# Kernel tuning notes

Measured on AMD Instinct MI355X. Metric: run time of the kernel, lower is better.

The kernel has to match this reference:

```python
import jax, jax.numpy as jnp
import numpy as np

# tree structure: B trees, layer sizes per tree 2048 -> 256 -> 32 -> 1 (arities 8, 8, 32)
B = 256
N0, N1, N2, N3 = B * 2048, B * 256, B * 32, B * 1
D_IN, HID, OUT = 128, 256, 10
EPS = 1e-5


def _bn(x, g, b):
    # BatchNorm1d, training-mode batch stats (biased variance), as in torch
    mu = jnp.mean(x, axis=0)
    var = jnp.var(x, axis=0)
    return (x - mu) * jax.lax.rsqrt(var + EPS) * g + b


def _tree_layer(pooled, w1, b1, bn1g, bn1b, w2, b2, bng, bnb):
    # MLP(2 layers): Linear -> BN -> ReLU -> Linear, then outer BN -> ReLU (next_layer)
    z = jax.nn.relu(_bn(pooled @ w1 + b1, bn1g, bn1b))
    z = z @ w2 + b2
    return jax.nn.relu(_bn(z, bng, bnb))


def setup_inputs() -> dict:
    key = jax.random.key(0)
    ks = jax.random.split(key, 12)
    s = 0.05
    ar = lambda n: jnp.arange(n, dtype=jnp.int32)
    inp = {
        'x': jax.random.normal(ks[0], (N0, D_IN), jnp.float32),
        # child -> parent index (global, trees are contiguous blocks)
        'parent1': ar(N0) // 8,
        'parent2': ar(N1) // 8,
        'parent3': ar(N2) // 32,
        # node -> tree id per layer (for sum tree-pooling readout)
        'tree0': ar(N0) // 2048,
        'tree1': ar(N1) // 256,
        'tree2': ar(N2) // 32,
        # layer 1 MLP (input_dim -> hidden)
        'l1_w1': jax.random.normal(ks[1], (D_IN, HID), jnp.float32) * s,
        'l1_b1': jnp.zeros((HID,), jnp.float32),
        'l1_bn1g': jnp.ones((HID,), jnp.float32),
        'l1_bn1b': jnp.zeros((HID,), jnp.float32),
        'l1_w2': jax.random.normal(ks[2], (HID, HID), jnp.float32) * s,
        'l1_b2': jnp.zeros((HID,), jnp.float32),
        'l1_bng': jnp.ones((HID,), jnp.float32),
        'l1_bnb': jnp.zeros((HID,), jnp.float32),
        # layers 2 and 3 MLPs (hidden -> hidden), stacked on axis 0
        'lw1': jax.random.normal(ks[3], (2, HID, HID), jnp.float32) * s,
        'lb1': jnp.zeros((2, HID), jnp.float32),
        'lbn1g': jnp.ones((2, HID), jnp.float32),
        'lbn1b': jnp.zeros((2, HID), jnp.float32),
        'lw2': jax.random.normal(ks[4], (2, HID, HID), jnp.float32) * s,
        'lb2': jnp.zeros((2, HID), jnp.float32),
        'lbng': jnp.ones((2, HID), jnp.float32),
        'lbnb': jnp.zeros((2, HID), jnp.float32),
        # prediction heads
        'pred0_w': jax.random.normal(ks[5], (D_IN, OUT), jnp.float32) * s,
        'pred0_b': jnp.zeros((OUT,), jnp.float32),
        'predh_w': jax.random.normal(ks[6], (3, HID, OUT), jnp.float32) * s,
        'predh_b': jnp.zeros((3, OUT), jnp.float32),
    }
    return inp


def reference(x, parent1, parent2, parent3, tree0, tree1, tree2,
              l1_w1, l1_b1, l1_bn1g, l1_bn1b, l1_w2, l1_b2, l1_bng, l1_bnb,
              lw1, lb1, lbn1g, lbn1b, lw2, lb2, lbng, lbnb,
              pred0_w, pred0_b, predh_w, predh_b):
    seg = jax.ops.segment_sum
    h0 = x
    # layer 1: sparse child pooling (spmm == segment_sum) + MLP + BN + ReLU
    h1 = _tree_layer(seg(h0, parent1, num_segments=N1),
                     l1_w1, l1_b1, l1_bn1g, l1_bn1b, l1_w2, l1_b2, l1_bng, l1_bnb)
    h2 = _tree_layer(seg(h1, parent2, num_segments=N2),
                     lw1[0], lb1[0], lbn1g[0], lbn1b[0], lw2[0], lb2[0], lbng[0], lbnb[0])
    h3 = _tree_layer(seg(h2, parent3, num_segments=N3),
                     lw1[1], lb1[1], lbn1g[1], lbn1b[1], lw2[1], lb2[1], lbng[1], lbnb[1])
    # sum tree-pooling readout over layers 0..depth-1, plus root-layer linear
    score = seg(h0, tree0, num_segments=B) @ pred0_w + pred0_b
    score = score + seg(h1, tree1, num_segments=B) @ predh_w[0] + predh_b[0]
    score = score + seg(h2, tree2, num_segments=B) @ predh_w[1] + predh_b[1]
    score = score + h3 @ predh_w[2] + predh_b[2]  # h3 has 1 root per tree -> [B, OUT]
    return score
```

## Files before the change

kernel.cpp:

```cpp
#include <hip/hip_runtime.h>
#include <hip/hip_bf16.h>


#define N0 (256*2048)
#define N1 (256*256)
#define N2 (256*32)
#define NB 256
#define BN_EPS 1e-5f

typedef __attribute__((ext_vector_type(8))) __bf16 bf16x8;
typedef __attribute__((ext_vector_type(8))) unsigned short u16x8;
typedef __attribute__((ext_vector_type(4))) unsigned short u16x4;
typedef __attribute__((ext_vector_type(4))) float f32x4;

__device__ inline float bf2f(unsigned short b) {
    unsigned u = ((unsigned)b) << 16;
    float f; __builtin_memcpy(&f, &u, 4); return f;
}
__device__ inline unsigned short f2bf(float f) {
    unsigned u; __builtin_memcpy(&u, &f, 4);
    u += 0x7fff + ((u >> 16) & 1);
    return (unsigned short)(u >> 16);
}

__global__ __launch_bounds__(256) void prep_weights(const float* __restrict__ l1_w1,
                                                    const float* __restrict__ l1_w2,
                                                    const float* __restrict__ lw1,
                                                    const float* __restrict__ lw2,
                                                    unsigned short* __restrict__ Wt) {
    int idx = blockIdx.x * 256 + threadIdx.x;
    if (idx >= 360448) return;
    float v;
    if (idx < 32768) {
        int n = idx >> 7, k = idx & 127;
        v = l1_w1[k * 256 + n];
    } else if (idx < 98304) {
        int j = idx - 32768, n = j >> 8, k = j & 255;
        v = l1_w2[k * 256 + n];
    } else if (idx < 163840) {
        int j = idx - 98304, n = j >> 8, k = j & 255;
        v = lw1[k * 256 + n];
    } else if (idx < 229376) {
        int j = idx - 163840, n = j >> 8, k = j & 255;
        v = lw2[k * 256 + n];
    } else if (idx < 294912) {
        int j = idx - 229376, n = j >> 8, k = j & 255;
        v = lw1[65536 + k * 256 + n];
    } else {
        int j = idx - 294912, n = j >> 8, k = j & 255;
        v = lw2[65536 + k * 256 + n];
    }
    Wt[idx] = f2bf(v);
}

__global__ __launch_bounds__(256) void pool8_128(const float* __restrict__ x,
                                                 unsigned short* __restrict__ out) {
    int v = blockIdx.x * 256 + threadIdx.x;
    int c4 = v & 31, p = v >> 5;
    const f32x4* xp = reinterpret_cast<const f32x4*>(x + (size_t)p * 8 * 128 + c4 * 4);
    f32x4 s = {0.f, 0.f, 0.f, 0.f};
#pragma unroll
    for (int c = 0; c < 8; ++c) s += xp[c * 32];
    u16x4 o;
#pragma unroll
    for (int e = 0; e < 4; ++e) o[e] = f2bf(s[e]);
    *reinterpret_cast<u16x4*>(out + (size_t)p * 128 + c4 * 4) = o;
}

template <int ROWS, int D>
__global__ void treesum_bf(const unsigned short* __restrict__ in, float* __restrict__ out) {
    int t = blockIdx.x, d = threadIdx.x;
    const unsigned short* p = in + (size_t)t * ROWS * D + d;
    float s = 0.f;
    for (int r = 0; r < ROWS; ++r) s += bf2f(p[(size_t)r * D]);
    out[t * D + d] = s;
}

template <int GROUP>
__global__ __launch_bounds__(256) void pool_bn_relu(const unsigned short* __restrict__ Z,
                                                    const float* __restrict__ scale,
                                                    const float* __restrict__ shift,
                                                    unsigned short* __restrict__ out) {
    int v = blockIdx.x * 256 + threadIdx.x;
    int c8 = v & 31, p = v >> 5;
    int d0 = c8 * 8;
    float sc[8], sh[8], s[8];
#pragma unroll
    for (int e = 0; e < 8; ++e) { sc[e] = scale[d0 + e]; sh[e] = shift[d0 + e]; s[e] = 0.f; }
#pragma unroll
    for (int g = 0; g < GROUP; ++g) {
        u16x8 z = *reinterpret_cast<const u16x8*>(Z + ((size_t)p * GROUP + g) * 256 + d0);
#pragma unroll
        for (int e = 0; e < 8; ++e) {
            float f = sc[e] * bf2f(z[e]) + sh[e];
            s[e] += f > 0.f ? f : 0.f;
        }
    }
    u16x8 o;
#pragma unroll
    for (int e = 0; e < 8; ++e) o[e] = f2bf(s[e]);
    *reinterpret_cast<u16x8*>(out + (size_t)p * 256 + d0) = o;
}

__global__ void bn_finalize(const float* __restrict__ partials,
                            const float* __restrict__ g, const float* __restrict__ b,
                            float invM, float* __restrict__ ss ) {
    int d = threadIdx.x;
    float s = 0.f, s2 = 0.f;
    for (int slot = 0; slot < 32; ++slot) {
        s  += partials[slot * 512 + d];
        s2 += partials[slot * 512 + 256 + d];
    }
    float mean = s * invM;
    float var = s2 * invM - mean * mean;
    float sc = g[d] * rsqrtf(var + BN_EPS);
    ss[d] = sc;
    ss[256 + d] = b[d] - mean * sc;
}

template <int KD, bool BN_A>
__global__ __launch_bounds__(256) void mfma_gemm(const unsigned short* __restrict__ A,
                                                 const float* __restrict__ scale,
                                                 const float* __restrict__ shift,
                                                 const unsigned short* __restrict__ Wt,
                                                 const float* __restrict__ bias,
                                                 unsigned short* __restrict__ C,
                                                 float* __restrict__ stat_partials) {
    constexpr int LDA = 72;
    __shared__ unsigned short Asb[64 * LDA];
    __shared__ unsigned short Bsb[256 * LDA];
    const int m0 = blockIdx.x * 64;
    const int tid = threadIdx.x;
    const int wave = tid >> 6, lane = tid & 63;
    const int q = lane >> 4, r = lane & 15;

    f32x4 acc[4][4];
#pragma unroll
    for (int i = 0; i < 4; ++i)
#pragma unroll
        for (int j = 0; j < 4; ++j) acc[i][j] = (f32x4){0.f, 0.f, 0.f, 0.f};

    for (int k0 = 0; k0 < KD; k0 += 64) {
#pragma unroll
        for (int i = 0; i < 2; ++i) {
            int v = tid + i * 256;
            int row = v >> 3, kc = v & 7;
            u16x8 d = *reinterpret_cast<const u16x8*>(A + (size_t)(m0 + row) * KD + k0 + kc * 8);
            if (BN_A) {
                u16x8 o;
#pragma unroll
                for (int e = 0; e < 8; ++e) {
                    int k = k0 + kc * 8 + e;
                    float f = scale[k] * bf2f(d[e]) + shift[k];
                    o[e] = f2bf(f > 0.f ? f : 0.f);
                }
                d = o;
            }
            *reinterpret_cast<u16x8*>(&Asb[row * LDA + kc * 8]) = d;
        }
#pragma unroll
        for (int i = 0; i < 8; ++i) {
            int v = tid + i * 256;
            int n = v >> 3, kc = v & 7;
            u16x8 d = *reinterpret_cast<const u16x8*>(Wt + (size_t)n * KD + k0 + kc * 8);
            *reinterpret_cast<u16x8*>(&Bsb[n * LDA + kc * 8]) = d;
        }
        __syncthreads();
#pragma unroll
        for (int s = 0; s < 2; ++s) {
            bf16x8 a[4], b[4];
#pragma unroll
            for (int i = 0; i < 4; ++i)
                a[i] = *reinterpret_cast<const bf16x8*>(&Asb[(i * 16 + r) * LDA + s * 32 + q * 8]);
#pragma unroll
            for (int j = 0; j < 4; ++j)
                b[j] = *reinterpret_cast<const bf16x8*>(&Bsb[(wave * 64 + j * 16 + r) * LDA + s * 32 + q * 8]);
#pragma unroll
            for (int i = 0; i < 4; ++i)
#pragma unroll
                for (int j = 0; j < 4; ++j)
                    acc[i][j] = __builtin_amdgcn_mfma_f32_16x16x32_bf16(a[i], b[j], acc[i][j], 0, 0, 0);
        }
        __syncthreads();
    }

    const int col_base = wave * 64;
    float sj[4], s2j[4];
#pragma unroll
    for (int j = 0; j < 4; ++j) {
        float bj = bias[col_base + j * 16 + r];
        float s = 0.f, s2 = 0.f;
#pragma unroll
        for (int i = 0; i < 4; ++i)
#pragma unroll
            for (int e = 0; e < 4; ++e) {
                acc[i][j][e] += bj;
                float v = acc[i][j][e];
                s += v; s2 += v * v;
            }
        s  += __shfl_xor(s, 16);  s  += __shfl_xor(s, 32);
        s2 += __shfl_xor(s2, 16); s2 += __shfl_xor(s2, 32);
        sj[j] = s; s2j[j] = s2;
    }
#pragma unroll
    for (int i = 0; i < 4; ++i)
#pragma unroll
        for (int e = 0; e < 4; ++e) {
            size_t row = m0 + i * 16 + q * 4 + e;
#pragma unroll
            for (int j = 0; j < 4; ++j)
                C[row * 256 + col_base + j * 16 + r] = f2bf(acc[i][j][e]);
        }
    if (q == 0) {
        int slot = blockIdx.x & 31;
#pragma unroll
        for (int j = 0; j < 4; ++j) {
            int col = col_base + j * 16 + r;
            atomicAdd(&stat_partials[slot * 512 + col], sj[j]);
            atomicAdd(&stat_partials[slot * 512 + 256 + col], s2j[j]);
        }
    }
}

__global__ __launch_bounds__(256) void head_kernel(const float* __restrict__ ts0,
                                                   const float* __restrict__ ts1,
                                                   const unsigned short* __restrict__ p3,
                                                   const unsigned short* __restrict__ Z3b,
                                                   const float* __restrict__ ss5,
                                                   const float* __restrict__ p0w,
                                                   const float* __restrict__ p0b,
                                                   const float* __restrict__ phw,
                                                   const float* __restrict__ phb,
                                                   float* __restrict__ out) {
    int t = blockIdx.x, d = threadIdx.x;
    float acc[10];
#pragma unroll
    for (int o = 0; o < 10; ++o) acc[o] = 0.f;
    if (d < 128) {
        float v = ts0[t * 128 + d];
#pragma unroll
        for (int o = 0; o < 10; ++o) acc[o] += v * p0w[d * 10 + o];
    }
    {
        float v = ts1[t * 256 + d];
#pragma unroll
        for (int o = 0; o < 10; ++o) acc[o] += v * phw[d * 10 + o];
    }
    {
        float v = bf2f(p3[t * 256 + d]);
#pragma unroll
        for (int o = 0; o < 10; ++o) acc[o] += v * phw[2560 + d * 10 + o];
    }
    {
        float v = ss5[d] * bf2f(Z3b[t * 256 + d]) + ss5[256 + d];
        v = v > 0.f ? v : 0.f;
#pragma unroll
        for (int o = 0; o < 10; ++o) acc[o] += v * phw[5120 + d * 10 + o];
    }
    __shared__ float red[256];
    for (int o = 0; o < 10; ++o) {
        red[d] = acc[o];
        __syncthreads();
        for (int s = 128; s > 0; s >>= 1) {
            if (d < s) red[d] += red[d + s];
            __syncthreads();
        }
        if (d == 0) out[t * 10 + o] = red[0] + p0b[o] + phb[o] + phb[10 + o] + phb[20 + o];
        __syncthreads();
    }
}

extern "C" void kernel_launch(void* const* d_in, const int* in_sizes, int n_in,
                              void* d_out, int out_size, void* d_ws, size_t ws_size,
                              hipStream_t stream) {
    const float* x       = (const float*)d_in[0];
    const float* l1_w1   = (const float*)d_in[7];
    const float* l1_b1   = (const float*)d_in[8];
    const float* l1_bn1g = (const float*)d_in[9];
    const float* l1_bn1b = (const float*)d_in[10];
    const float* l1_w2   = (const float*)d_in[11];
    const float* l1_b2   = (const float*)d_in[12];
    const float* l1_bng  = (const float*)d_in[13];
    const float* l1_bnb  = (const float*)d_in[14];
    const float* lw1     = (const float*)d_in[15];
    const float* lb1     = (const float*)d_in[16];
    const float* lbn1g   = (const float*)d_in[17];
    const float* lbn1b   = (const float*)d_in[18];
    const float* lw2     = (const float*)d_in[19];
    const float* lb2     = (const float*)d_in[20];
    const float* lbng    = (const float*)d_in[21];
    const float* lbnb    = (const float*)d_in[22];
    const float* pred0_w = (const float*)d_in[23];
    const float* pred0_b = (const float*)d_in[24];
    const float* predh_w = (const float*)d_in[25];
    const float* predh_b = (const float*)d_in[26];
    float* out = (float*)d_out;

    uint8_t* wsb = (uint8_t*)d_ws;
    unsigned short* pooled1 = (unsigned short*)(wsb);
    unsigned short* Z1      = (unsigned short*)(wsb + (16ull << 20));
    unsigned short* Z2      = (unsigned short*)(wsb + (48ull << 20));
    unsigned short* pooled2 = (unsigned short*)(wsb + (80ull << 20));
    unsigned short* Z2a     = (unsigned short*)(wsb + (84ull << 20));
    unsigned short* Z2b     = (unsigned short*)(wsb + (88ull << 20));
    unsigned short* pooled3 = (unsigned short*)(wsb + (92ull << 20));
    unsigned short* Z3a     = (unsigned short*)(wsb + (92ull << 20) + 131072);
    unsigned short* Z3b     = (unsigned short*)(wsb + (92ull << 20) + 262144);
    unsigned short* Wt      = (unsigned short*)(wsb + (93ull << 20));
    float* ts0   = (float*)(wsb + (94ull << 20));
    float* ts1   = (float*)(wsb + (94ull << 20) + 131072);
    float* stats = (float*)(wsb + (95ull << 20));

    auto SP = [&](int i) { return stats + i * 16384; };
    float* ssbase = stats + 6 * 16384;
    auto SS = [&](int i) { return ssbase + i * 512; };

    hipMemsetAsync(stats, 0, 6 * 16384 * sizeof(float), stream);
    prep_weights<<<1408, 256, 0, stream>>>(l1_w1, l1_w2, lw1, lw2, Wt);

    pool8_128<<<N1 * 32 / 256, 256, 0, stream>>>(x, pooled1);
    treesum_bf<256, 128><<<NB, 128, 0, stream>>>(pooled1, ts0);
    mfma_gemm<128, false><<<N1 / 64, 256, 0, stream>>>(pooled1, nullptr, nullptr,
                                                       Wt, l1_b1, Z1, SP(0));
    bn_finalize<<<1, 256, 0, stream>>>(SP(0), l1_bn1g, l1_bn1b, 1.f / N1, SS(0));
    mfma_gemm<256, true><<<N1 / 64, 256, 0, stream>>>(Z1, SS(0), SS(0) + 256,
                                                      Wt + 32768, l1_b2, Z2, SP(1));
    bn_finalize<<<1, 256, 0, stream>>>(SP(1), l1_bng, l1_bnb, 1.f / N1, SS(1));
    pool_bn_relu<8><<<N2 * 32 / 256, 256, 0, stream>>>(Z2, SS(1), SS(1) + 256, pooled2);
    treesum_bf<32, 256><<<NB, 256, 0, stream>>>(pooled2, ts1);

    mfma_gemm<256, false><<<N2 / 64, 256, 0, stream>>>(pooled2, nullptr, nullptr,
                                                       Wt + 98304, lb1, Z2a, SP(2));
    bn_finalize<<<1, 256, 0, stream>>>(SP(2), lbn1g, lbn1b, 1.f / N2, SS(2));
    mfma_gemm<256, true><<<N2 / 64, 256, 0, stream>>>(Z2a, SS(2), SS(2) + 256,
                                                      Wt + 163840, lb2, Z2b, SP(3));
    bn_finalize<<<1, 256, 0, stream>>>(SP(3), lbng, lbnb, 1.f / N2, SS(3));
    pool_bn_relu<32><<<NB * 32 / 256, 256, 0, stream>>>(Z2b, SS(3), SS(3) + 256, pooled3);

    mfma_gemm<256, false><<<NB / 64, 256, 0, stream>>>(pooled3, nullptr, nullptr,
                                                       Wt + 229376, lb1 + 256, Z3a, SP(4));
    bn_finalize<<<1, 256, 0, stream>>>(SP(4), lbn1g + 256, lbn1b + 256, 1.f / NB, SS(4));
    mfma_gemm<256, true><<<NB / 64, 256, 0, stream>>>(Z3a, SS(4), SS(4) + 256,
                                                      Wt + 294912, lb2 + 256, Z3b, SP(5));
    bn_finalize<<<1, 256, 0, stream>>>(SP(5), lbng + 256, lbnb + 256, 1.f / NB, SS(5));

    head_kernel<<<NB, 256, 0, stream>>>(ts0, ts1, pooled3, Z3b, SS(5),
                                        pred0_w, pred0_b, predh_w, predh_b, out);
}
```

Baseline: 190.3 us.

## Fuse BN finalize and tree-sum readouts into neighbouring kernels, retile big GEMMs

Removes the separate bn_finalize launches by recomputing scale/shift from partial stats in each consumer kernel's prologue, and folds the per-tree sum readouts into the pooling kernels using block reductions plus atomics. The stat partial slots are reduced from 32 to 8 so the prologue reads less. The layer-1 GEMMs use 128-row tiles with 512 threads to reuse the weight tile across more rows. This trades fewer launches and passes for redundant per-block BN finalize work and more atomic contention.

```diff
diff --git a/kernel.cpp b/kernel.cpp
--- a/kernel.cpp
+++ b/kernel.cpp
@@ -7,6 +7,7 @@
 #define N2 (256*32)
 #define NB 256
 #define BN_EPS 1e-5f
+#define NSLOT 8
 
 typedef __attribute__((ext_vector_type(8))) __bf16 bf16x8;
 typedef __attribute__((ext_vector_type(8))) unsigned short u16x8;
@@ -53,10 +54,31 @@
     Wt[idx] = f2bf(v);
 }
 
+__device__ inline void bn_prologue(int tid, const float* __restrict__ partials,
+                                   const float* __restrict__ g, const float* __restrict__ b,
+                                   float invM, float* sc_lds, float* sh_lds) {
+    if (tid < 256) {
+        float s = 0.f, s2 = 0.f;
+#pragma unroll
+        for (int k = 0; k < NSLOT; ++k) {
+            s  += partials[k * 512 + tid];
+            s2 += partials[k * 512 + 256 + tid];
+        }
+        float mean = s * invM;
+        float var = s2 * invM - mean * mean;
+        float sc = g[tid] * rsqrtf(var + BN_EPS);
+        sc_lds[tid] = sc;
+        sh_lds[tid] = b[tid] - mean * sc;
+    }
+}
+
 __global__ __launch_bounds__(256) void pool8_128(const float* __restrict__ x,
-                                                 unsigned short* __restrict__ out) {
-    int v = blockIdx.x * 256 + threadIdx.x;
-    int c4 = v & 31, p = v >> 5;
+                                                 unsigned short* __restrict__ out,
+                                                 float* __restrict__ ts0) {
+    int tid = threadIdx.x;
+    int c4 = tid & 31, pl = tid >> 5;
+    int p = blockIdx.x * 8 + pl;
+    int tree = blockIdx.x >> 5;
     const f32x4* xp = reinterpret_cast<const f32x4*>(x + (size_t)p * 8 * 128 + c4 * 4);
     f32x4 s = {0.f, 0.f, 0.f, 0.f};
 #pragma unroll
@@ -65,31 +87,44 @@
 #pragma unroll
     for (int e = 0; e < 4; ++e) o[e] = f2bf(s[e]);
     *reinterpret_cast<u16x4*>(out + (size_t)p * 128 + c4 * 4) = o;
-}
-
-template <int ROWS, int D>
-__global__ void treesum_bf(const unsigned short* __restrict__ in, float* __restrict__ out) {
-    int t = blockIdx.x, d = threadIdx.x;
-    const unsigned short* p = in + (size_t)t * ROWS * D + d;
-    float s = 0.f;
-    for (int r = 0; r < ROWS; ++r) s += bf2f(p[(size_t)r * D]);
-    out[t * D + d] = s;
-}
-
-template <int GROUP>
+    __shared__ float red[4][32][4];
+    int w = tid >> 6;
+    f32x4 t = s;
+#pragma unroll
+    for (int e = 0; e < 4; ++e) t[e] += __shfl_xor(t[e], 32);
+    if ((tid & 63) < 32) {
+#pragma unroll
+        for (int e = 0; e < 4; ++e) red[w][c4][e] = t[e];
+    }
+    __syncthreads();
+    if (tid < 128) {
+        int cc = tid >> 2, e = tid & 3;
+        float v = red[0][cc][e] + red[1][cc][e] + red[2][cc][e] + red[3][cc][e];
+        atomicAdd(&ts0[tree * 128 + tid], v);
+    }
+}
+
+template <int GROUP, bool TS>
 __global__ __launch_bounds__(256) void pool_bn_relu(const unsigned short* __restrict__ Z,
-                                                    const float* __restrict__ scale,
-                                                    const float* __restrict__ shift,
-                                                    unsigned short* __restrict__ out) {
-    int v = blockIdx.x * 256 + threadIdx.x;
-    int c8 = v & 31, p = v >> 5;
+                                                    const float* __restrict__ partials,
+                                                    const float* __restrict__ g,
+                                                    const float* __restrict__ b,
+                                                    float invM,
+                                                    unsigned short* __restrict__ out,
+                                                    float* __restrict__ ts) {
+    __shared__ float sc_lds[256], sh_lds[256];
+    int tid = threadIdx.x;
+    bn_prologue(tid, partials, g, b, invM, sc_lds, sh_lds);
+    __syncthreads();
+    int c8 = tid & 31, pl = tid >> 5;
+    size_t p = (size_t)blockIdx.x * 8 + pl;
     int d0 = c8 * 8;
     float sc[8], sh[8], s[8];
 #pragma unroll
-    for (int e = 0; e < 8; ++e) { sc[e] = scale[d0 + e]; sh[e] = shift[d0 + e]; s[e] = 0.f; }
-#pragma unroll
-    for (int g = 0; g < GROUP; ++g) {
-        u16x8 z = *reinterpret_cast<const u16x8*>(Z + ((size_t)p * GROUP + g) * 256 + d0);
+    for (int e = 0; e < 8; ++e) { sc[e] = sc_lds[d0 + e]; sh[e] = sh_lds[d0 + e]; s[e] = 0.f; }
+#pragma unroll
+    for (int gi = 0; gi < GROUP; ++gi) {
+        u16x8 z = *reinterpret_cast<const u16x8*>(Z + (p * GROUP + gi) * 256 + d0);
 #pragma unroll
         for (int e = 0; e < 8; ++e) {
             float f = sc[e] * bf2f(z[e]) + sh[e];
@@ -99,40 +134,50 @@
     u16x8 o;
 #pragma unroll
     for (int e = 0; e < 8; ++e) o[e] = f2bf(s[e]);
-    *reinterpret_cast<u16x8*>(out + (size_t)p * 256 + d0) = o;
-}
-
-__global__ void bn_finalize(const float* __restrict__ partials,
-                            const float* __restrict__ g, const float* __restrict__ b,
-                            float invM, float* __restrict__ ss ) {
-    int d = threadIdx.x;
-    float s = 0.f, s2 = 0.f;
-    for (int slot = 0; slot < 32; ++slot) {
-        s  += partials[slot * 512 + d];
-        s2 += partials[slot * 512 + 256 + d];
-    }
-    float mean = s * invM;
-    float var = s2 * invM - mean * mean;
-    float sc = g[d] * rsqrtf(var + BN_EPS);
-    ss[d] = sc;
-    ss[256 + d] = b[d] - mean * sc;
-}
-
-template <int KD, bool BN_A>
-__global__ __launch_bounds__(256) void mfma_gemm(const unsigned short* __restrict__ A,
-                                                 const float* __restrict__ scale,
-                                                 const float* __restrict__ shift,
-                                                 const unsigned short* __restrict__ Wt,
-                                                 const float* __restrict__ bias,
-                                                 unsigned short* __restrict__ C,
-                                                 float* __restrict__ stat_partials) {
+    *reinterpret_cast<u16x8*>(out + p * 256 + d0) = o;
+    if (TS) {
+        __shared__ float red[4][32][8];
+        int tree = blockIdx.x >> 2;
+        int w = tid >> 6;
+#pragma unroll
+        for (int e = 0; e < 8; ++e) s[e] += __shfl_xor(s[e], 32);
+        if ((tid & 63) < 32) {
+#pragma unroll
+            for (int e = 0; e < 8; ++e) red[w][c8][e] = s[e];
+        }
+        __syncthreads();
+        {
+            int cc = tid >> 3, e = tid & 7;
+            float v = red[0][cc][e] + red[1][cc][e] + red[2][cc][e] + red[3][cc][e];
+            atomicAdd(&ts[tree * 256 + tid], v);
+        }
+    }
+}
+
+template <int KD, bool BN_A, int BM>
+__global__ __launch_bounds__(BM * 4) void mfma_gemm(const unsigned short* __restrict__ A,
+                                                    const float* __restrict__ partials_in,
+                                                    const float* __restrict__ bn_g,
+                                                    const float* __restrict__ bn_b,
+                                                    float invM,
+                                                    const unsigned short* __restrict__ Wt,
+                                                    const float* __restrict__ bias,
+                                                    unsigned short* __restrict__ C,
+                                                    float* __restrict__ stat_partials) {
     constexpr int LDA = 72;
-    __shared__ unsigned short Asb[64 * LDA];
+    constexpr int NT = BM * 4;
+    __shared__ unsigned short Asb[BM * LDA];
     __shared__ unsigned short Bsb[256 * LDA];
-    const int m0 = blockIdx.x * 64;
+    __shared__ float sc_lds[256], sh_lds[256];
     const int tid = threadIdx.x;
+    if (BN_A) {
+        bn_prologue(tid, partials_in, bn_g, bn_b, invM, sc_lds, sh_lds);
+        __syncthreads();
+    }
+    const int m0 = blockIdx.x * BM;
     const int wave = tid >> 6, lane = tid & 63;
     const int q = lane >> 4, r = lane & 15;
+    const int wc = wave & 3, wr = wave >> 2;
 
     f32x4 acc[4][4];
 #pragma unroll
@@ -143,7 +188,7 @@
     for (int k0 = 0; k0 < KD; k0 += 64) {
 #pragma unroll
         for (int i = 0; i < 2; ++i) {
-            int v = tid + i * 256;
+            int v = tid + i * NT;
             int row = v >> 3, kc = v & 7;
             u16x8 d = *reinterpret_cast<const u16x8*>(A + (size_t)(m0 + row) * KD + k0 + kc * 8);
             if (BN_A) {
@@ -151,7 +196,7 @@
 #pragma unroll
                 for (int e = 0; e < 8; ++e) {
                     int k = k0 + kc * 8 + e;
-                    float f = scale[k] * bf2f(d[e]) + shift[k];
+                    float f = sc_lds[k] * bf2f(d[e]) + sh_lds[k];
                     o[e] = f2bf(f > 0.f ? f : 0.f);
                 }
                 d = o;
@@ -159,8 +204,8 @@
             *reinterpret_cast<u16x8*>(&Asb[row * LDA + kc * 8]) = d;
         }
 #pragma unroll
-        for (int i = 0; i < 8; ++i) {
-            int v = tid + i * 256;
+        for (int i = 0; i < 2048 / NT; ++i) {
+            int v = tid + i * NT;
             int n = v >> 3, kc = v & 7;
             u16x8 d = *reinterpret_cast<const u16x8*>(Wt + (size_t)n * KD + k0 + kc * 8);
             *reinterpret_cast<u16x8*>(&Bsb[n * LDA + kc * 8]) = d;
@@ -171,10 +216,10 @@
             bf16x8 a[4], b[4];
 #pragma unroll
             for (int i = 0; i < 4; ++i)
-                a[i] = *reinterpret_cast<const bf16x8*>(&Asb[(i * 16 + r) * LDA + s * 32 + q * 8]);
+                a[i] = *reinterpret_cast<const bf16x8*>(&Asb[(wr * 64 + i * 16 + r) * LDA + s * 32 + q * 8]);
 #pragma unroll
             for (int j = 0; j < 4; ++j)
-                b[j] = *reinterpret_cast<const bf16x8*>(&Bsb[(wave * 64 + j * 16 + r) * LDA + s * 32 + q * 8]);
+                b[j] = *reinterpret_cast<const bf16x8*>(&Bsb[(wc * 64 + j * 16 + r) * LDA + s * 32 + q * 8]);
 #pragma unroll
             for (int i = 0; i < 4; ++i)
 #pragma unroll
@@ -184,11 +229,10 @@
         __syncthreads();
     }
 
-    const int col_base = wave * 64;
     float sj[4], s2j[4];
 #pragma unroll
     for (int j = 0; j < 4; ++j) {
-        float bj = bias[col_base + j * 16 + r];
+        float bj = bias[wc * 64 + j * 16 + r];
         float s = 0.f, s2 = 0.f;
 #pragma unroll
         for (int i = 0; i < 4; ++i)
@@ -206,16 +250,16 @@
     for (int i = 0; i < 4; ++i)
 #pragma unroll
         for (int e = 0; e < 4; ++e) {
-            size_t row = m0 + i * 16 + q * 4 + e;
+            size_t row = m0 + wr * 64 + i * 16 + q * 4 + e;
 #pragma unroll
             for (int j = 0; j < 4; ++j)
-                C[row * 256 + col_base + j * 16 + r] = f2bf(acc[i][j][e]);
+                C[row * 256 + wc * 64 + j * 16 + r] = f2bf(acc[i][j][e]);
         }
     if (q == 0) {
-        int slot = blockIdx.x & 31;
+        int slot = blockIdx.x & (NSLOT - 1);
 #pragma unroll
         for (int j = 0; j < 4; ++j) {
-            int col = col_base + j * 16 + r;
+            int col = wc * 64 + j * 16 + r;
             atomicAdd(&stat_partials[slot * 512 + col], sj[j]);
             atomicAdd(&stat_partials[slot * 512 + 256 + col], s2j[j]);
         }
@@ -226,13 +270,19 @@
                                                    const float* __restrict__ ts1,
                                                    const unsigned short* __restrict__ p3,
                                                    const unsigned short* __restrict__ Z3b,
-                                                   const float* __restrict__ ss5,
+                                                   const float* __restrict__ partials,
+                                                   const float* __restrict__ g,
+                                                   const float* __restrict__ b,
+                                                   float invM,
                                                    const float* __restrict__ p0w,
                                                    const float* __restrict__ p0b,
                                                    const float* __restrict__ phw,
                                                    const float* __restrict__ phb,
                                                    float* __restrict__ out) {
+    __shared__ float sc_lds[256], sh_lds[256];
     int t = blockIdx.x, d = threadIdx.x;
+    bn_prologue(d, partials, g, b, invM, sc_lds, sh_lds);
+    __syncthreads();
     float acc[10];
 #pragma unroll
     for (int o = 0; o < 10; ++o) acc[o] = 0.f;
@@ -252,7 +302,7 @@
         for (int o = 0; o < 10; ++o) acc[o] += v * phw[2560 + d * 10 + o];
     }
     {
-        float v = ss5[d] * bf2f(Z3b[t * 256 + d]) + ss5[256 + d];
+        float v = sc_lds[d] * bf2f(Z3b[t * 256 + d]) + sh_lds[d];
         v = v > 0.f ? v : 0.f;
 #pragma unroll
         for (int o = 0; o < 10; ++o) acc[o] += v * phw[5120 + d * 10 + o];
@@ -307,43 +357,37 @@
     unsigned short* Z3a     = (unsigned short*)(wsb + (92ull << 20) + 131072);
     unsigned short* Z3b     = (unsigned short*)(wsb + (92ull << 20) + 262144);
     unsigned short* Wt      = (unsigned short*)(wsb + (93ull << 20));
-    float* ts0   = (float*)(wsb + (94ull << 20));
-    float* ts1   = (float*)(wsb + (94ull << 20) + 131072);
-    float* stats = (float*)(wsb + (95ull << 20));
-
-    auto SP = [&](int i) { return stats + i * 16384; };
-    float* ssbase = stats + 6 * 16384;
-    auto SS = [&](int i) { return ssbase + i * 512; };
-
-    hipMemsetAsync(stats, 0, 6 * 16384 * sizeof(float), stream);
+    float* zbase = (float*)(wsb + (94ull << 20));
+    float* ts0   = zbase;
+    float* ts1   = zbase + 32768;
+    float* stats = zbase + 32768 + 65536;
+    auto SP = [&](int i) { return stats + i * (NSLOT * 512); };
+    size_t zbytes = (32768 + 65536 + 6 * NSLOT * 512) * sizeof(float);
+
+    hipMemsetAsync(zbase, 0, zbytes, stream);
     prep_weights<<<1408, 256, 0, stream>>>(l1_w1, l1_w2, lw1, lw2, Wt);
 
-    pool8_128<<<N1 * 32 / 256, 256, 0, stream>>>(x, pooled1);
-    treesum_bf<256, 128><<<NB, 128, 0, stream>>>(pooled1, ts0);
-    mfma_gemm<128, false><<<N1 / 64, 256, 0, stream>>>(pooled1, nullptr, nullptr,
-                                                       Wt, l1_b1, Z1, SP(0));
-    bn_finalize<<<1, 256, 0, stream>>>(SP(0), l1_bn1g, l1_bn1b, 1.f / N1, SS(0));
-    mfma_gemm<256, true><<<N1 / 64, 256, 0, stream>>>(Z1, SS(0), SS(0) + 256,
-                                                      Wt + 32768, l1_b2, Z2, SP(1));
-    bn_finalize<<<1, 256, 0, stream>>>(SP(1), l1_bng, l1_bnb, 1.f / N1, SS(1));
-    pool_bn_relu<8><<<N2 * 32 / 256, 256, 0, stream>>>(Z2, SS(1), SS(1) + 256, pooled2);
-    treesum_bf<32, 256><<<NB, 256, 0, stream>>>(pooled2, ts1);
-
-    mfma_gemm<256, false><<<N2 / 64, 256, 0, stream>>>(pooled2, nullptr, nullptr,
-                                                       Wt + 98304, lb1, Z2a, SP(2));
-    bn_finalize<<<1, 256, 0, stream>>>(SP(2), lbn1g, lbn1b, 1.f / N2, SS(2));
-    mfma_gemm<256, true><<<N2 / 64, 256, 0, stream>>>(Z2a, SS(2), SS(2) + 256,
-                                                      Wt + 163840, lb2, Z2b, SP(3));
-    bn_finalize<<<1, 256, 0, stream>>>(SP(3), lbng, lbnb, 1.f / N2, SS(3));
-    pool_bn_relu<32><<<NB * 32 / 256, 256, 0, stream>>>(Z2b, SS(3), SS(3) + 256, pooled3);
-
-    mfma_gemm<256, false><<<NB / 64, 256, 0, stream>>>(pooled3, nullptr, nullptr,
-                                                       Wt + 229376, lb1 + 256, Z3a, SP(4));
-    bn_finalize<<<1, 256, 0, stream>>>(SP(4), lbn1g + 256, lbn1b + 256, 1.f / NB, SS(4));
-    mfma_gemm<256, true><<<NB / 64, 256, 0, stream>>>(Z3a, SS(4), SS(4) + 256,
-                                                      Wt + 294912, lb2 + 256, Z3b, SP(5));
-    bn_finalize<<<1, 256, 0, stream>>>(SP(5), lbng + 256, lbnb + 256, 1.f / NB, SS(5));
-
-    head_kernel<<<NB, 256, 0, stream>>>(ts0, ts1, pooled3, Z3b, SS(5),
+    pool8_128<<<N1 / 8, 256, 0, stream>>>(x, pooled1, ts0);
+    mfma_gemm<128, false, 128><<<N1 / 128, 512, 0, stream>>>(
+        pooled1, nullptr, nullptr, nullptr, 0.f, Wt, l1_b1, Z1, SP(0));
+    mfma_gemm<256, true, 128><<<N1 / 128, 512, 0, stream>>>(
+        Z1, SP(0), l1_bn1g, l1_bn1b, 1.f / N1, Wt + 32768, l1_b2, Z2, SP(1));
+    pool_bn_relu<8, true><<<N2 / 8, 256, 0, stream>>>(
+        Z2, SP(1), l1_bng, l1_bnb, 1.f / N1, pooled2, ts1);
+
+    mfma_gemm<256, false, 64><<<N2 / 64, 256, 0, stream>>>(
+        pooled2, nullptr, nullptr, nullptr, 0.f, Wt + 98304, lb1, Z2a, SP(2));
+    mfma_gemm<256, true, 64><<<N2 / 64, 256, 0, stream>>>(
+        Z2a, SP(2), lbn1g, lbn1b, 1.f / N2, Wt + 163840, lb2, Z2b, SP(3));
+    pool_bn_relu<32, false><<<NB / 8, 256, 0, stream>>>(
+        Z2b, SP(3), lbng, lbnb, 1.f / N2, pooled3, nullptr);
+
+    mfma_gemm<256, false, 64><<<NB / 64, 256, 0, stream>>>(
+        pooled3, nullptr, nullptr, nullptr, 0.f, Wt + 229376, lb1 + 256, Z3a, SP(4));
+    mfma_gemm<256, true, 64><<<NB / 64, 256, 0, stream>>>(
+        Z3a, SP(4), lbn1g + 256, lbn1b + 256, 1.f / NB, Wt + 294912, lb2 + 256, Z3b, SP(5));
+
+    head_kernel<<<NB, 256, 0, stream>>>(ts0, ts1, pooled3, Z3b, SP(5),
+                                        lbng + 256, lbnb + 256, 1.f / NB,
                                         pred0_w, pred0_b, predh_w, predh_b, out);
 }
```

Result: slower. 196.9 us (+3.5%).
